# Optimization experiments

Measured on AMD Instinct MI355X. Metric: run time of the kernel, lower is better.

The kernel has to match this reference:

```python
import jax, jax.numpy as jnp
import numpy as np

IN_DIM, H1, H2, H3, LATENT = 1024, 1024, 512, 256, 256
D, K, BETA = 32, 2048, 0.25
B = 16384


def _leaky(x):
    return jax.nn.leaky_relu(x, negative_slope=0.01)


def setup_inputs() -> dict:
    key = jax.random.key(0)
    ks = jax.random.split(key, 18)
    def lin(k, fan_in, fan_out):
        kw, kb = jax.random.split(k)
        s = 1.0 / np.sqrt(fan_in)
        W = jax.random.uniform(kw, (fan_in, fan_out), jnp.float32, -s, s)
        b = jax.random.uniform(kb, (fan_out,), jnp.float32, -s, s)
        return W, b
    We1, be1 = lin(ks[0], IN_DIM, H1)
    We2, be2 = lin(ks[1], H1, H2)
    We3, be3 = lin(ks[2], H2, H3)
    We4, be4 = lin(ks[3], H3, LATENT)
    Wd1, bd1 = lin(ks[4], LATENT, H3)
    Wd2, bd2 = lin(ks[5], H3, H2)
    Wd3, bd3 = lin(ks[6], H2, H1)
    Wd4, bd4 = lin(ks[7], H1, IN_DIM)
    E = jax.random.uniform(ks[8], (K, D), jnp.float32, -1.0 / K, 1.0 / K)  # codebook
    x = jax.random.uniform(ks[9], (B, IN_DIM), jnp.float32)
    return {"x": x, "We1": We1, "be1": be1, "We2": We2, "be2": be2,
            "We3": We3, "be3": be3, "We4": We4, "be4": be4, "E": E,
            "Wd1": Wd1, "bd1": bd1, "Wd2": Wd2, "bd2": bd2,
            "Wd3": Wd3, "bd3": bd3, "Wd4": Wd4, "bd4": bd4}


def reference(x, We1, be1, We2, be2, We3, be3, We4, be4, E,
              Wd1, bd1, Wd2, bd2, Wd3, bd3, Wd4, bd4):
    # encoder MLP
    h = _leaky(x @ We1 + be1)
    h = _leaky(h @ We2 + be2)
    h = _leaky(h @ We3 + be3)
    z = h @ We4 + be4                      # [B, LATENT]
    # vector quantizer
    zr = z.reshape(-1, D)                  # [N, D], N = B*LATENT/D
    dist = (jnp.sum(zr * zr, axis=1, keepdims=True)
            + jnp.sum(E * E, axis=1)
            - 2.0 * zr @ E.T)              # [N, K]
    idx = jnp.argmin(dist, axis=1)         # [N]
    # one-hot @ E == direct gather of nearest codebook rows
    q = E[idx].reshape(z.shape)            # [B, LATENT]
    commit = jnp.mean(jnp.sum(jnp.square(jax.lax.stop_gradient(q) - z), axis=1))
    embed = jnp.mean(jnp.sum(jnp.square(q - jax.lax.stop_gradient(z)), axis=1))
    vq_loss = BETA * commit + embed
    e = z + jax.lax.stop_gradient(q - z)   # straight-through
    # decoder MLP
    h = _leaky(e @ Wd1 + bd1)
    h = _leaky(h @ Wd2 + bd2)
    h = _leaky(h @ Wd3 + bd3)
    recon = jax.nn.sigmoid(h @ Wd4 + bd4)
    recon_loss = jnp.mean(jnp.sum(jnp.square(recon - x), axis=-1))
    loss = recon_loss + vq_loss
    return z, e, recon, loss, recon_loss, vq_loss
```

## Files before the change

kernel.cpp:

```cpp
#include <hip/hip_runtime.h>
#include <stdint.h>

typedef __attribute__((ext_vector_type(8))) _Float16 half8;
typedef __attribute__((ext_vector_type(4))) _Float16 half4;
typedef __attribute__((ext_vector_type(4))) float f32x4;

__device__ __forceinline__ void gload_lds16(const void* g, void* l) {
  __builtin_amdgcn_global_load_lds(
      (const __attribute__((address_space(1))) void*)g,
      (__attribute__((address_space(3))) void*)l, 16, 0, 0);
}

#define GBAR asm volatile("s_barrier" ::: "memory")
#define LGKM0                                            \
  asm volatile("s_waitcnt lgkmcnt(0)" ::: "memory");     \
  __builtin_amdgcn_sched_barrier(0)

#define MMA_Q(QM, QN)                                                        \
  __builtin_amdgcn_s_setprio(1);                                             \
  _Pragma("unroll") for (int s = 0; s < 2; s++)                              \
  _Pragma("unroll") for (int i = 0; i < 4; i++)                              \
  _Pragma("unroll") for (int j = 0; j < 2; j++)                              \
      acc[(QM) * 4 + i][(QN) * 2 + j] = __builtin_amdgcn_mfma_f32_16x16x32_f16( \
          af[i][s], bq[j][s], acc[(QM) * 4 + i][(QN) * 2 + j], 0, 0, 0);     \
  __builtin_amdgcn_s_setprio(0);

template <int EPI>
__global__ __launch_bounds__(512, 2) void gemm8p(
    const _Float16* __restrict__ A, const _Float16* __restrict__ Bt,
    const float* __restrict__ bias, _Float16* __restrict__ Ch,
    float* __restrict__ Cf, int M, int N, int Kd,
    const _Float16* __restrict__ Xref, float* __restrict__ lossAcc) {
  extern __shared__ __align__(16) char dyn[];

  const int tid = threadIdx.x;
  const int lane = tid & 63;
  const int wav = tid >> 6;
  const int wr = wav >> 2;
  const int wc = wav & 3;
  const int l15 = lane & 15;
  const int quad = lane >> 4;

  const int nx = gridDim.x;
  const int nwg = nx * (int)gridDim.y;
  int bid = (int)blockIdx.y * nx + (int)blockIdx.x;
  bid = (bid & 7) * (nwg >> 3) + (bid >> 3);
  const int shift = 31 - __clz(nx);
  const int m0 = (bid >> shift) * 256;
  const int n0 = (bid & (nx - 1)) * 256;

  f32x4 acc[8][4];
#pragma unroll
  for (int i = 0; i < 8; i++)
#pragma unroll
    for (int j = 0; j < 4; j++) acc[i][j] = (f32x4){0.f, 0.f, 0.f, 0.f};

  auto stageA = [&](int kt, int slot, int RB) {
    const int row = RB + (tid >> 3);
    const int ch = tid & 7;
    const int gm = m0 + ((row >> 6) & 1) * 128 + (row >> 7) * 64 + (row & 63);
    const int kc = (ch ^ (row & 7)) << 3;
    gload_lds16(A + (size_t)gm * Kd + kt + kc,
                dyn + slot * 65536 + row * 128 + ch * 16);
  };
  auto stageB = [&](int kt, int slot, int RB) {
    const int row = RB + (tid >> 3);
    const int ch = tid & 7;
    const int gn = n0 + ((row >> 5) & 3) * 64 + (row >> 7) * 32 + (row & 31);
    const int kc = (ch ^ (row & 7)) << 3;
    gload_lds16(Bt + (size_t)gn * Kd + kt + kc,
                dyn + slot * 65536 + 32768 + row * 128 + ch * 16);
  };

  half8 af[4][2], bq[2][2];
  auto dsA = [&](const _Float16* As, int qm) {
#pragma unroll
    for (int i = 0; i < 4; i++) {
      const int ra = qm * 128 + wr * 64 + i * 16 + l15;
#pragma unroll
      for (int s = 0; s < 2; s++)
        af[i][s] = *(const half8*)&As[ra * 64 + (((s * 4 + quad) ^ (ra & 7)) << 3)];
    }
  };
  auto dsB = [&](const _Float16* Bs, int qn) {
#pragma unroll
    for (int j = 0; j < 2; j++) {
      const int rb = qn * 128 + wc * 32 + j * 16 + l15;
#pragma unroll
      for (int s = 0; s < 2; s++)
        bq[j][s] = *(const half8*)&Bs[rb * 64 + (((s * 4 + quad) ^ (rb & 7)) << 3)];
    }
  };

  const int NT = Kd >> 6;

  stageA(0, 0, 0);
  stageA(0, 0, 64);
  stageB(0, 0, 128);
  stageB(0, 0, 192);
  stageA(0, 0, 128);
  stageA(0, 0, 192);
  stageB(0, 0, 0);
  stageB(0, 0, 64);
  stageA(64, 1, 0);
  stageA(64, 1, 64);
  stageB(64, 1, 128);
  stageB(64, 1, 192);
  asm volatile("s_waitcnt vmcnt(4)" ::: "memory");
  GBAR;

  for (int t = 0; t < NT; ++t) {
    const int slot = t & 1;
    const int nsl = slot ^ 1;
    const int kt1 = (t + 1) << 6;
    const int kt2 = (t + 2) << 6;
    const bool p1 = (t + 1) < NT;
    const bool p2 = (t + 2) < NT;
    const _Float16* As = (const _Float16*)(dyn + slot * 65536);
    const _Float16* Bs = (const _Float16*)(dyn + slot * 65536 + 32768);

    dsA(As, 0);
    dsB(Bs, 0);
    if (p1) { stageA(kt1, nsl, 128); stageA(kt1, nsl, 192); }
    GBAR;
    LGKM0;
    MMA_Q(0, 0);
    GBAR;
    dsB(Bs, 1);
    if (p1) { stageB(kt1, nsl, 0); stageB(kt1, nsl, 64); }
    GBAR;
    LGKM0;
    MMA_Q(0, 1);
    GBAR;
    dsA(As, 1);
    if (p2) { stageA(kt2, slot, 0); stageA(kt2, slot, 64); }
    GBAR;
    LGKM0;
    MMA_Q(1, 1);
    GBAR;
    dsB(Bs, 0);
    if (p2) { stageB(kt2, slot, 128); stageB(kt2, slot, 192); }
    GBAR;
    LGKM0;
    MMA_Q(1, 0);
    if (p2) {
      asm volatile("s_waitcnt vmcnt(4)" ::: "memory");
    } else {
      asm volatile("s_waitcnt vmcnt(0)" ::: "memory");
    }
    GBAR;
  }

  float lsum = 0.f;
  float* eb = (float*)dyn;
  float* red = (float*)dyn + 64 * 256;
#pragma unroll
  for (int p = 0; p < 4; p++) {
    __syncthreads();
    if (wr == (p >> 1)) {
#pragma unroll
      for (int mi2 = 0; mi2 < 4; mi2++) {
        const int mi = (p & 1) * 4 + mi2;
#pragma unroll
        for (int ni = 0; ni < 4; ni++)
#pragma unroll
          for (int r = 0; r < 4; r++) {
            const int rl = mi2 * 16 + quad * 4 + r;
            const int cl = wc * 64 + ni * 16 + l15;
            eb[rl * 256 + cl] = acc[mi][ni][r];
          }
      }
    }
    __syncthreads();
#pragma unroll
    for (int j = 0; j < 8; j++) {
      const int c = j * 512 + tid;
      const int rl = c >> 6;
      const int cl = (c & 63) * 4;
      const f32x4 v = *(const f32x4*)&eb[rl * 256 + cl];
      const int gcol = n0 + cl;
      const f32x4 bv = *(const f32x4*)&bias[gcol];
      const size_t o = (size_t)(m0 + p * 64 + rl) * N + gcol;
      if (EPI == 0) {
        half4 h;
#pragma unroll
        for (int q = 0; q < 4; q++) {
          float tv = v[q] + bv[q];
          tv = tv > 0.f ? tv : 0.01f * tv;
          h[q] = (_Float16)tv;
        }
        *(half4*)&Ch[o] = h;
      } else {
        const half4 xr = *(const half4*)&Xref[o];
        f32x4 sv;
#pragma unroll
        for (int q = 0; q < 4; q++) {
          const float sg = 1.f / (1.f + __expf(-(v[q] + bv[q])));
          sv[q] = sg;
          const float d = sg - (float)xr[q];
          lsum += d * d;
        }
        *(f32x4*)&Cf[o] = sv;
      }
    }
  }
  if (EPI == 2) {
    __syncthreads();
    red[tid] = lsum;
    __syncthreads();
    for (int s = 256; s > 0; s >>= 1) {
      if (tid < s) red[tid] += red[tid + s];
      __syncthreads();
    }
    if (tid == 0) atomicAdd(lossAcc, red[0]);
  }
}

template <int EPI, int BM, int BN>
__global__ __launch_bounds__(256, ((BM + BN) >= 256 ? 2 : ((BM + BN) == 192 ? 3 : 4)))
void gemm_bt(
    const _Float16* __restrict__ A, const _Float16* __restrict__ Bt,
    const float* __restrict__ bias, _Float16* __restrict__ Ch,
    float* __restrict__ Cf, int M, int N, int Kd,
    const _Float16* __restrict__ Xref, float* __restrict__ lossAcc) {
  constexpr int WM = BM / 2, WN = BN / 2;
  constexpr int MF = WM / 16, NF = WN / 16;
  constexpr int CA = BM / 32, CB = BN / 32;
  constexpr int CHUNKS = CA + CB;
  constexpr int STAGE = (BM + BN) * 64;
  __shared__ __align__(16) _Float16 smem[2 * STAGE];
  float* red = (float*)smem + 64 * BN;

  const int tid = threadIdx.x;
  const int lane = tid & 63;
  const int wav = tid >> 6;
  const int nx = gridDim.x;
  const int nwg = nx * (int)gridDim.y;
  int bid = (int)blockIdx.y * nx + (int)blockIdx.x;
  bid = (bid & 7) * (nwg >> 3) + (bid >> 3);
  const int shift = 31 - __clz(nx);
  const int m0 = (bid >> shift) * BM;
  const int n0 = (bid & (nx - 1)) * BN;
  const int wm = (wav >> 1) * WM;
  const int wn = (wav & 1) * WN;
  const int l15 = lane & 15;
  const int quad = lane >> 4;

  f32x4 acc[MF][NF];
#pragma unroll
  for (int i = 0; i < MF; i++)
#pragma unroll
    for (int j = 0; j < NF; j++) acc[i][j] = (f32x4){0.f, 0.f, 0.f, 0.f};

  auto issue = [&](int kt, int b) {
    _Float16* As = smem + b * STAGE;
    _Float16* Bs = As + BM * 64;
#pragma unroll
    for (int j = 0; j < CA; j++) {
      const int ci = j * 256 + tid;
      const int row = ci >> 3;
      const int kc = ((ci & 7) ^ (row & 7)) << 3;
      gload_lds16(A + (size_t)(m0 + row) * Kd + kt + kc, &As[ci * 8]);
    }
#pragma unroll
    for (int j = 0; j < CB; j++) {
      const int ci = j * 256 + tid;
      const int row = ci >> 3;
      const int kc = ((ci & 7) ^ (row & 7)) << 3;
      gload_lds16(Bt + (size_t)(n0 + row) * Kd + kt + kc, &Bs[ci * 8]);
    }
  };

  int buf = 0;
  issue(0, 0);
  for (int kt = 0; kt < Kd; kt += 64) {
    if (kt + 64 < Kd) {
      issue(kt + 64, buf ^ 1);
      asm volatile("s_waitcnt vmcnt(%0)" ::"i"(CHUNKS) : "memory");
    } else {
      asm volatile("s_waitcnt vmcnt(0)" ::: "memory");
    }
    asm volatile("s_barrier" ::: "memory");

    const _Float16* As = smem + buf * STAGE;
    const _Float16* Bs = As + BM * 64;
#pragma unroll
    for (int s = 0; s < 2; s++) {
      half8 af[MF], bqv[NF];
#pragma unroll
      for (int i = 0; i < MF; i++) {
        const int ra = wm + i * 16 + l15;
        const int ca = (s * 4 + quad) ^ (ra & 7);
        af[i] = *(const half8*)&As[ra * 64 + ca * 8];
      }
#pragma unroll
      for (int i = 0; i < NF; i++) {
        const int rb = wn + i * 16 + l15;
        const int cb = (s * 4 + quad) ^ (rb & 7);
        bqv[i] = *(const half8*)&Bs[rb * 64 + cb * 8];
      }
#pragma unroll
      for (int mi = 0; mi < MF; mi++)
#pragma unroll
        for (int ni = 0; ni < NF; ni++)
          acc[mi][ni] = __builtin_amdgcn_mfma_f32_16x16x32_f16(af[mi], bqv[ni],
                                                               acc[mi][ni], 0, 0, 0);
    }
    asm volatile("s_barrier" ::: "memory");
    buf ^= 1;
  }

  float lsum = 0.f;
  float* eb = (float*)smem;
  constexpr int DIV = BN / 4;
#pragma unroll
  for (int p = 0; p < BM / 64; p++) {
    __syncthreads();
    if ((wm >> 6) == p) {
#pragma unroll
      for (int mi = 0; mi < MF; mi++)
#pragma unroll
        for (int ni = 0; ni < NF; ni++)
#pragma unroll
          for (int r = 0; r < 4; r++) {
            const int rl = (wm & 63) + mi * 16 + quad * 4 + r;
            const int cl = wn + ni * 16 + l15;
            eb[rl * BN + cl] = acc[mi][ni][r];
          }
    }
    __syncthreads();
#pragma unroll
    for (int j = 0; j < BN / 16; j++) {
      const int c = j * 256 + tid;
      const int rl = c / DIV;
      const int cl = (c % DIV) * 4;
      const f32x4 v = *(const f32x4*)&eb[rl * BN + cl];
      const int gcol = n0 + cl;
      const f32x4 bv = *(const f32x4*)&bias[gcol];
      const size_t o = (size_t)(m0 + p * 64 + rl) * N + gcol;
      if (EPI == 0) {
        half4 h;
#pragma unroll
        for (int q = 0; q < 4; q++) {
          float t = v[q] + bv[q];
          t = t > 0.f ? t : 0.01f * t;
          h[q] = (_Float16)t;
        }
        *(half4*)&Ch[o] = h;
      } else if (EPI == 1) {
        f32x4 t;
        half4 h;
#pragma unroll
        for (int q = 0; q < 4; q++) {
          t[q] = v[q] + bv[q];
          h[q] = (_Float16)t[q];
        }
        *(f32x4*)&Cf[o] = t;
        *(half4*)&Ch[o] = h;
      } else {
        const half4 xr = *(const half4*)&Xref[o];
        f32x4 sv;
#pragma unroll
        for (int q = 0; q < 4; q++) {
          const float s = 1.f / (1.f + __expf(-(v[q] + bv[q])));
          sv[q] = s;
          const float d = s - (float)xr[q];
          lsum += d * d;
        }
        *(f32x4*)&Cf[o] = sv;
      }
    }
  }
  if (EPI == 2) {
    __syncthreads();
    red[tid] = lsum;
    __syncthreads();
    for (int s = 128; s > 0; s >>= 1) {
      if (tid < s) red[tid] += red[tid + s];
      __syncthreads();
    }
    if (tid == 0) atomicAdd(lossAcc, red[0]);
  }
}

__global__ __launch_bounds__(256, 4) void vq_argmin(
    const _Float16* __restrict__ zh, const _Float16* __restrict__ Ehf,
    const float* __restrict__ E, const float* __restrict__ ek2,
    float* __restrict__ e_out, _Float16* __restrict__ eh_out,
    float* __restrict__ vq_acc) {
  __shared__ __align__(16) _Float16 Es[512 * 32];
  __shared__ float ek2s[512];
  __shared__ float z2s[128];
  __shared__ int idxs[128];
  __shared__ float vred[256];

  const int tid = threadIdx.x;
  const int lane = tid & 63;
  const int wav = tid >> 6;
  const int l15 = lane & 15;
  const int quad = lane >> 4;
  const int rbase = blockIdx.x * 128 + wav * 32;
  constexpr unsigned KEYMASK = 0xFFFFF800u;

  half8 zf[2];
  float z2p[2];
#pragma unroll
  for (int m = 0; m < 2; m++) {
    zf[m] = *(const half8*)(zh + ((size_t)(rbase + m * 16 + l15)) * 32 + quad * 8);
    float s = 0.f;
#pragma unroll
    for (int j = 0; j < 8; j++) {
      float v = (float)zf[m][j];
      s += v * v;
    }
    s += __shfl_xor(s, 16);
    s += __shfl_xor(s, 32);
    z2p[m] = s;
  }
  if (quad == 0) {
#pragma unroll
    for (int m = 0; m < 2; m++) z2s[wav * 32 + m * 16 + l15] = z2p[m];
  }

  float key[2][4];
#pragma unroll
  for (int m = 0; m < 2; m++)
#pragma unroll
    for (int r = 0; r < 4; r++) key[m][r] = 1e30f;

  for (int cb = 0; cb < 2048; cb += 512) {
    __syncthreads();
#pragma unroll
    for (int j = 0; j < 8; j++) {
      const int u = j * 256 + tid;
      gload_lds16(Ehf + (size_t)cb * 32 + u * 8, &Es[u * 8]);
    }
    if (tid < 128) gload_lds16(&ek2[cb + tid * 4], &ek2s[tid * 4]);
    __syncthreads();

    int idxv = cb + l15;
    for (int c16 = 0; c16 < 32; c16++) {
      const half8 ef = *(const half8*)&Es[(c16 * 64 + lane) * 8];
      const float e2 = ek2s[c16 * 16 + l15];
      const f32x4 cinit = (f32x4){e2, e2, e2, e2};
      f32x4 d0 = __builtin_amdgcn_mfma_f32_16x16x32_f16(zf[0], ef, cinit, 0, 0, 0);
      f32x4 d1 = __builtin_amdgcn_mfma_f32_16x16x32_f16(zf[1], ef, cinit, 0, 0, 0);
#pragma unroll
      for (int r = 0; r < 4; r++) {
        key[0][r] = fminf(key[0][r],
                          __uint_as_float((__float_as_uint(d0[r]) & KEYMASK) | idxv));
        key[1][r] = fminf(key[1][r],
                          __uint_as_float((__float_as_uint(d1[r]) & KEYMASK) | idxv));
      }
      idxv += 16;
    }
  }

#pragma unroll
  for (int off = 1; off < 16; off <<= 1)
#pragma unroll
    for (int m = 0; m < 2; m++)
#pragma unroll
      for (int r = 0; r < 4; r++)
        key[m][r] = fminf(key[m][r], __shfl_xor(key[m][r], off));

  float vpart = 0.f;
  if (l15 == 0) {
#pragma unroll
    for (int m = 0; m < 2; m++)
#pragma unroll
      for (int r = 0; r < 4; r++) {
        const unsigned kb = __float_as_uint(key[m][r]);
        const int rl = wav * 32 + m * 16 + quad * 4 + r;
        idxs[rl] = (int)(kb & 0x7FFu);
        vpart += z2s[rl] + __uint_as_float(kb & KEYMASK);
      }
  }
  vred[tid] = vpart;
  __syncthreads();
  for (int s = 128; s > 0; s >>= 1) {
    if (tid < s) vred[tid] += vred[tid + s];
    __syncthreads();
  }
  if (tid == 0) atomicAdd(vq_acc, vred[0]);

#pragma unroll
  for (int it = 0; it < 2; it++) {
    const int slot = it * 256 + tid;
    const int rowb = slot >> 2, part = slot & 3;
    const int idx = idxs[rowb];
    const size_t orow = ((size_t)blockIdx.x * 128 + rowb) * 32 + part * 8;
    const f32x4 ea = *(const f32x4*)(E + (size_t)idx * 32 + part * 8);
    const f32x4 ebv = *(const f32x4*)(E + (size_t)idx * 32 + part * 8 + 4);
    *(f32x4*)(e_out + orow) = ea;
    *(f32x4*)(e_out + orow + 4) = ebv;
    half8 ehv;
#pragma unroll
    for (int j = 0; j < 4; j++) {
      ehv[j] = (_Float16)ea[j];
      ehv[j + 4] = (_Float16)ebv[j];
    }
    *(half8*)(eh_out + orow) = ehv;
  }
}

struct PrepArgs {
  const float* W[8];
  _Float16* Wt[8];
  int Kw[8], Nw[8];
  int base[9];
  const float* x;
  _Float16* xh;
  const float* E;
  _Float16* Ehf;
  float* ek2;
};

__global__ __launch_bounds__(256) void prep_k(PrepArgs a) {
  __shared__ float t[32][33];
  const int b = blockIdx.x;
  const int tid = threadIdx.x;
  if (b < 8192) {
    const size_t i = (size_t)b * 256 + tid;
    const f32x4 va = *(const f32x4*)(a.x + i * 8);
    const f32x4 vb = *(const f32x4*)(a.x + i * 8 + 4);
    half8 h;
#pragma unroll
    for (int j = 0; j < 4; j++) {
      h[j] = (_Float16)va[j];
      h[j + 4] = (_Float16)vb[j];
    }
    *(half8*)(a.xh + i * 8) = h;
    return;
  }
  if (b < 8192 + 3456) {
    int l = b - 8192;
    int w = 0;
    while (l >= a.base[w + 1]) w++;
    l -= a.base[w];
    const float* W = a.W[w];
    _Float16* Wt = a.Wt[w];
    const int K = a.Kw[w], N = a.Nw[w];
    const int nb = N >> 5;
    const int bx = (l % nb) * 32, by = (l / nb) * 32;
    const int tx = tid & 31, ty = tid >> 5;
#pragma unroll
    for (int i = 0; i < 32; i += 8)
      t[ty + i][tx] = W[(size_t)(by + ty + i) * N + bx + tx];
    __syncthreads();
#pragma unroll
    for (int i = 0; i < 32; i += 8)
      Wt[(size_t)(bx + ty + i) * K + by + tx] = (_Float16)t[tx][ty + i];
    return;
  }
  const int c = (b - 8192 - 3456) * 256 + tid;
  float s = 0.f;
#pragma unroll
  for (int k = 0; k < 32; k++) {
    const float v = a.E[(size_t)c * 32 + k];
    s += v * v;
    a.Ehf[(size_t)((c >> 4) * 64 + (k >> 3) * 16 + (c & 15)) * 8 + (k & 7)] =
        (_Float16)(-2.f * v);
  }
  a.ek2[c] = s;
}

__global__ void finalize_k(const float* __restrict__ scal, float* __restrict__ out) {
  const float vq = 1.25f * (scal[0] / 16384.f);
  const float rl = scal[1] / 16384.f;
  out[0] = rl + vq;
  out[1] = rl;
  out[2] = vq;
}

extern "C" void kernel_launch(void* const* d_in, const int* in_sizes, int n_in,
                              void* d_out, int out_size, void* d_ws, size_t ws_size,
                              hipStream_t stream) {
  const float* x = (const float*)d_in[0];
  const float* be1 = (const float*)d_in[2];
  const float* be2 = (const float*)d_in[4];
  const float* be3 = (const float*)d_in[6];
  const float* be4 = (const float*)d_in[8];
  const float* E = (const float*)d_in[9];
  const float* bd1 = (const float*)d_in[11];
  const float* bd2 = (const float*)d_in[13];
  const float* bd3 = (const float*)d_in[15];
  const float* bd4 = (const float*)d_in[17];

  float* out = (float*)d_out;
  char* ws = (char*)d_ws;

  size_t off = 0;
  auto alloc = [&](size_t bytes) {
    size_t r = off;
    off += (bytes + 255) & ~(size_t)255;
    return r;
  };
  const size_t oXH = alloc((size_t)16384 * 1024 * 2);
  const size_t oWT1 = alloc((size_t)1024 * 1024 * 2);
  const size_t oWT2 = alloc((size_t)512 * 1024 * 2);
  const size_t oWT3 = alloc((size_t)256 * 512 * 2);
  const size_t oWT4 = alloc((size_t)256 * 256 * 2);
  const size_t oWD1 = alloc((size_t)256 * 256 * 2);
  const size_t oWD2 = alloc((size_t)512 * 256 * 2);
  const size_t oWD3 = alloc((size_t)1024 * 512 * 2);
  const size_t oWD4 = alloc((size_t)1024 * 1024 * 2);
  const size_t oEHF = alloc((size_t)2048 * 32 * 2);
  const size_t oEK2 = alloc((size_t)2048 * 4);
  const size_t oSC = alloc(256);
  const size_t oZH = alloc((size_t)16384 * 256 * 2);
  const size_t oQH = alloc((size_t)16384 * 256 * 2);
  const size_t oH1 = alloc((size_t)16384 * 1024 * 2);
  const size_t oH2 = alloc((size_t)16384 * 512 * 2);
  const size_t oH3 = alloc((size_t)16384 * 256 * 2);

  _Float16* xh = (_Float16*)(ws + oXH);
  _Float16* WT1 = (_Float16*)(ws + oWT1);
  _Float16* WT2 = (_Float16*)(ws + oWT2);
  _Float16* WT3 = (_Float16*)(ws + oWT3);
  _Float16* WT4 = (_Float16*)(ws + oWT4);
  _Float16* WD1 = (_Float16*)(ws + oWD1);
  _Float16* WD2 = (_Float16*)(ws + oWD2);
  _Float16* WD3 = (_Float16*)(ws + oWD3);
  _Float16* WD4 = (_Float16*)(ws + oWD4);
  _Float16* Ehf = (_Float16*)(ws + oEHF);
  float* ek2 = (float*)(ws + oEK2);
  float* scal = (float*)(ws + oSC);
  _Float16* zhw = (_Float16*)(ws + oZH);
  _Float16* qh = (_Float16*)(ws + oQH);
  _Float16* h1 = (_Float16*)(ws + oH1);
  _Float16* h2 = (_Float16*)(ws + oH2);
  _Float16* h3 = (_Float16*)(ws + oH3);

  float* zout = out;
  float* eout = out + (size_t)16384 * 256;
  float* rout = out + (size_t)16384 * 256 * 2;
  float* sout = rout + (size_t)16384 * 1024;

  hipMemsetAsync(ws + oSC, 0, 8, stream);

  hipFuncSetAttribute((const void*)gemm8p<0>,
                      hipFuncAttributeMaxDynamicSharedMemorySize, 131072);
  hipFuncSetAttribute((const void*)gemm8p<2>,
                      hipFuncAttributeMaxDynamicSharedMemorySize, 131072);

  PrepArgs pa;
  pa.W[0] = (const float*)d_in[1];  pa.Wt[0] = WT1; pa.Kw[0] = 1024; pa.Nw[0] = 1024;
  pa.W[1] = (const float*)d_in[3];  pa.Wt[1] = WT2; pa.Kw[1] = 1024; pa.Nw[1] = 512;
  pa.W[2] = (const float*)d_in[5];  pa.Wt[2] = WT3; pa.Kw[2] = 512;  pa.Nw[2] = 256;
  pa.W[3] = (const float*)d_in[7];  pa.Wt[3] = WT4; pa.Kw[3] = 256;  pa.Nw[3] = 256;
  pa.W[4] = (const float*)d_in[10]; pa.Wt[4] = WD1; pa.Kw[4] = 256;  pa.Nw[4] = 256;
  pa.W[5] = (const float*)d_in[12]; pa.Wt[5] = WD2; pa.Kw[5] = 256;  pa.Nw[5] = 512;
  pa.W[6] = (const float*)d_in[14]; pa.Wt[6] = WD3; pa.Kw[6] = 512;  pa.Nw[6] = 1024;
  pa.W[7] = (const float*)d_in[16]; pa.Wt[7] = WD4; pa.Kw[7] = 1024; pa.Nw[7] = 1024;
  int acc = 0;
  for (int w = 0; w < 8; w++) {
    pa.base[w] = acc;
    acc += (pa.Kw[w] >> 5) * (pa.Nw[w] >> 5);
  }
  pa.base[8] = acc;
  pa.x = x; pa.xh = xh; pa.E = E; pa.Ehf = Ehf; pa.ek2 = ek2;

  dim3 blk(256);
  prep_k<<<8192 + 3456 + 8, blk, 0, stream>>>(pa);

  gemm8p<0><<<dim3(4, 64), dim3(512), 131072, stream>>>(
      xh, WT1, be1, h1, nullptr, 16384, 1024, 1024, nullptr, nullptr);
  gemm_bt<0, 128, 128><<<dim3(4, 128), blk, 0, stream>>>(
      h1, WT2, be2, h2, nullptr, 16384, 512, 1024, nullptr, nullptr);
  gemm_bt<0, 64, 64><<<dim3(4, 256), blk, 0, stream>>>(
      h2, WT3, be3, h3, nullptr, 16384, 256, 512, nullptr, nullptr);
  gemm_bt<1, 64, 64><<<dim3(4, 256), blk, 0, stream>>>(
      h3, WT4, be4, zhw, zout, 16384, 256, 256, nullptr, nullptr);
  vq_argmin<<<1024, blk, 0, stream>>>(zhw, Ehf, E, ek2, eout, qh, &scal[0]);
  gemm_bt<0, 64, 64><<<dim3(4, 256), blk, 0, stream>>>(
      qh, WD1, bd1, h3, nullptr, 16384, 256, 256, nullptr, nullptr);
  gemm_bt<0, 128, 128><<<dim3(4, 128), blk, 0, stream>>>(
      h3, WD2, bd2, h2, nullptr, 16384, 512, 256, nullptr, nullptr);
  gemm8p<0><<<dim3(4, 64), dim3(512), 131072, stream>>>(
      h2, WD3, bd3, h1, nullptr, 16384, 1024, 512, nullptr, nullptr);
  gemm8p<2><<<dim3(4, 64), dim3(512), 131072, stream>>>(
      h1, WD4, bd4, nullptr, rout, 16384, 1024, 1024, xh, &scal[1]);
  finalize_k<<<1, 1, 0, stream>>>(scal, sout);
}
```

Baseline: 381.7 us.

## Reorder GEMM prefetch stages, peel last K-iteration, and prefetch Xref during final MMAs

Changes the order in which A and B quarter-tiles are staged into LDS so more loads stay in flight (vmcnt 6 instead of 4), and peels the final K iteration out of the main loop. In the peeled iteration, for the sigmoid/loss epilogue, the reference input tiles are loaded into registers while the last MFMAs run, so the epilogue no longer waits on those global loads. This uses 32 extra half4 registers per thread, which raises register pressure and may lower occupancy.

```diff
diff --git a/kernel.cpp b/kernel.cpp
--- a/kernel.cpp
+++ b/kernel.cpp
@@ -94,60 +94,116 @@
 
   const int NT = Kd >> 6;
 
+  half4 xp[4][8];
+
   stageA(0, 0, 0);
   stageA(0, 0, 64);
-  stageB(0, 0, 128);
-  stageB(0, 0, 192);
   stageA(0, 0, 128);
   stageA(0, 0, 192);
   stageB(0, 0, 0);
   stageB(0, 0, 64);
+  stageB(0, 0, 128);
+  stageB(0, 0, 192);
   stageA(64, 1, 0);
   stageA(64, 1, 64);
   stageB(64, 1, 128);
   stageB(64, 1, 192);
-  asm volatile("s_waitcnt vmcnt(4)" ::: "memory");
+  stageA(64, 1, 128);
+  stageA(64, 1, 192);
+  asm volatile("s_waitcnt vmcnt(6)" ::: "memory");
   GBAR;
 
-  for (int t = 0; t < NT; ++t) {
+  for (int t = 0; t < NT - 1; ++t) {
     const int slot = t & 1;
     const int nsl = slot ^ 1;
     const int kt1 = (t + 1) << 6;
     const int kt2 = (t + 2) << 6;
-    const bool p1 = (t + 1) < NT;
-    const bool p2 = (t + 2) < NT;
+    const bool s2 = (t + 2) < NT;
     const _Float16* As = (const _Float16*)(dyn + slot * 65536);
     const _Float16* Bs = (const _Float16*)(dyn + slot * 65536 + 32768);
 
     dsA(As, 0);
     dsB(Bs, 0);
-    if (p1) { stageA(kt1, nsl, 128); stageA(kt1, nsl, 192); }
+    stageB(kt1, nsl, 0);
+    stageB(kt1, nsl, 64);
     GBAR;
     LGKM0;
     MMA_Q(0, 0);
     GBAR;
     dsB(Bs, 1);
-    if (p1) { stageB(kt1, nsl, 0); stageB(kt1, nsl, 64); }
+    if (s2) { stageA(kt2, slot, 0); stageA(kt2, slot, 64); }
     GBAR;
     LGKM0;
     MMA_Q(0, 1);
     GBAR;
     dsA(As, 1);
-    if (p2) { stageA(kt2, slot, 0); stageA(kt2, slot, 64); }
+    if (s2) { stageB(kt2, slot, 128); stageB(kt2, slot, 192); }
     GBAR;
     LGKM0;
     MMA_Q(1, 1);
     GBAR;
     dsB(Bs, 0);
-    if (p2) { stageB(kt2, slot, 128); stageB(kt2, slot, 192); }
+    if (s2) { stageA(kt2, slot, 128); stageA(kt2, slot, 192); }
     GBAR;
     LGKM0;
     MMA_Q(1, 0);
-    if (p2) {
-      asm volatile("s_waitcnt vmcnt(4)" ::: "memory");
+    if (s2) {
+      asm volatile("s_waitcnt vmcnt(6)" ::: "memory");
     } else {
       asm volatile("s_waitcnt vmcnt(0)" ::: "memory");
     }
+    GBAR;
+  }
+
+  {
+    const int slot = (NT - 1) & 1;
+    const _Float16* As = (const _Float16*)(dyn + slot * 65536);
+    const _Float16* Bs = (const _Float16*)(dyn + slot * 65536 + 32768);
+    const size_t xbase = (size_t)m0 * N + n0 + (size_t)wav * N + lane * 4;
+
+    dsA(As, 0);
+    dsB(Bs, 0);
+    if (EPI == 2) {
+#pragma unroll
+      for (int j = 0; j < 8; j++)
+        xp[0][j] = *(const half4*)&Xref[xbase + (size_t)(0 * 64 + j * 8) * N];
+    }
+    GBAR;
+    LGKM0;
+    MMA_Q(0, 0);
+    GBAR;
+
+    dsB(Bs, 1);
+    if (EPI == 2) {
+#pragma unroll
+      for (int j = 0; j < 8; j++)
+        xp[1][j] = *(const half4*)&Xref[xbase + (size_t)(1 * 64 + j * 8) * N];
+    }
+    GBAR;
+    LGKM0;
+    MMA_Q(0, 1);
+    GBAR;
+
+    dsA(As, 1);
+    if (EPI == 2) {
+#pragma unroll
+      for (int j = 0; j < 8; j++)
+        xp[2][j] = *(const half4*)&Xref[xbase + (size_t)(2 * 64 + j * 8) * N];
+    }
+    GBAR;
+    LGKM0;
+    MMA_Q(1, 1);
+    GBAR;
+
+    dsB(Bs, 0);
+    if (EPI == 2) {
+#pragma unroll
+      for (int j = 0; j < 8; j++)
+        xp[3][j] = *(const half4*)&Xref[xbase + (size_t)(3 * 64 + j * 8) * N];
+    }
+    GBAR;
+    LGKM0;
+    MMA_Q(1, 0);
     GBAR;
   }
 
@@ -191,7 +247,7 @@
         }
         *(half4*)&Ch[o] = h;
       } else {
-        const half4 xr = *(const half4*)&Xref[o];
+        const half4 xr = xp[p][j];
         f32x4 sv;
 #pragma unroll
         for (int q = 0; q < 4; q++) {
```

Measured after the change: 384.9 us. Within noise of the previous version (+0.8%).

## Deepen the GEMM prefetch schedule and store the sigmoid epilogue directly from registers

Applied to the files above, without the earlier changes.

The staged global-to-LDS loads are reordered so that more of the next-next K tile is issued earlier. The wait threshold rises from vmcnt(4) to vmcnt(6), which leaves more loads in flight behind the MFMA quarters. For the final sigmoid/loss GEMM, the epilogue no longer stages accumulators through LDS with per-pass barriers: each lane applies bias and sigmoid, then writes its fragment values straight to global memory and reads X in place. This removes LDS traffic and synchronisation, but in exchange it uses narrower, less coalesced scalar stores and loads, and it relies on the new per-fragment column mapping being correct.

```diff
diff --git a/kernel.cpp b/kernel.cpp
--- a/kernel.cpp
+++ b/kernel.cpp
@@ -96,17 +96,19 @@
 
   stageA(0, 0, 0);
   stageA(0, 0, 64);
-  stageB(0, 0, 128);
-  stageB(0, 0, 192);
   stageA(0, 0, 128);
   stageA(0, 0, 192);
   stageB(0, 0, 0);
   stageB(0, 0, 64);
+  stageB(0, 0, 128);
+  stageB(0, 0, 192);
   stageA(64, 1, 0);
   stageA(64, 1, 64);
   stageB(64, 1, 128);
   stageB(64, 1, 192);
-  asm volatile("s_waitcnt vmcnt(4)" ::: "memory");
+  stageA(64, 1, 128);
+  stageA(64, 1, 192);
+  asm volatile("s_waitcnt vmcnt(6)" ::: "memory");
   GBAR;
 
   for (int t = 0; t < NT; ++t) {
@@ -115,104 +117,115 @@
     const int kt1 = (t + 1) << 6;
     const int kt2 = (t + 2) << 6;
     const bool p1 = (t + 1) < NT;
-    const bool p2 = (t + 2) < NT;
+    const bool s2 = (t + 2) < NT;
     const _Float16* As = (const _Float16*)(dyn + slot * 65536);
     const _Float16* Bs = (const _Float16*)(dyn + slot * 65536 + 32768);
 
     dsA(As, 0);
     dsB(Bs, 0);
-    if (p1) { stageA(kt1, nsl, 128); stageA(kt1, nsl, 192); }
+    if (p1) { stageB(kt1, nsl, 0); stageB(kt1, nsl, 64); }
     GBAR;
     LGKM0;
     MMA_Q(0, 0);
     GBAR;
     dsB(Bs, 1);
-    if (p1) { stageB(kt1, nsl, 0); stageB(kt1, nsl, 64); }
+    if (s2) { stageA(kt2, slot, 0); stageA(kt2, slot, 64); }
     GBAR;
     LGKM0;
     MMA_Q(0, 1);
     GBAR;
     dsA(As, 1);
-    if (p2) { stageA(kt2, slot, 0); stageA(kt2, slot, 64); }
+    if (s2) { stageB(kt2, slot, 128); stageB(kt2, slot, 192); }
     GBAR;
     LGKM0;
     MMA_Q(1, 1);
     GBAR;
     dsB(Bs, 0);
-    if (p2) { stageB(kt2, slot, 128); stageB(kt2, slot, 192); }
+    if (s2) { stageA(kt2, slot, 128); stageA(kt2, slot, 192); }
     GBAR;
     LGKM0;
     MMA_Q(1, 0);
-    if (p2) {
-      asm volatile("s_waitcnt vmcnt(4)" ::: "memory");
+    if (s2) {
+      asm volatile("s_waitcnt vmcnt(6)" ::: "memory");
     } else {
       asm volatile("s_waitcnt vmcnt(0)" ::: "memory");
     }
     GBAR;
   }
 
-  float lsum = 0.f;
-  float* eb = (float*)dyn;
-  float* red = (float*)dyn + 64 * 256;
-#pragma unroll
-  for (int p = 0; p < 4; p++) {
-    __syncthreads();
-    if (wr == (p >> 1)) {
-#pragma unroll
-      for (int mi2 = 0; mi2 < 4; mi2++) {
-        const int mi = (p & 1) * 4 + mi2;
-#pragma unroll
-        for (int ni = 0; ni < 4; ni++)
-#pragma unroll
-          for (int r = 0; r < 4; r++) {
-            const int rl = mi2 * 16 + quad * 4 + r;
-            const int cl = wc * 64 + ni * 16 + l15;
-            eb[rl * 256 + cl] = acc[mi][ni][r];
-          }
-      }
-    }
-    __syncthreads();
-#pragma unroll
-    for (int j = 0; j < 8; j++) {
-      const int c = j * 512 + tid;
-      const int rl = c >> 6;
-      const int cl = (c & 63) * 4;
-      const f32x4 v = *(const f32x4*)&eb[rl * 256 + cl];
-      const int gcol = n0 + cl;
-      const f32x4 bv = *(const f32x4*)&bias[gcol];
-      const size_t o = (size_t)(m0 + p * 64 + rl) * N + gcol;
-      if (EPI == 0) {
+  if (EPI == 2) {
+    float lsum = 0.f;
+    int colv[4];
+    float bv[4];
+#pragma unroll
+    for (int ni = 0; ni < 4; ni++) {
+      colv[ni] = n0 + wc * 64 + (ni >> 1) * 32 + (ni & 1) * 16 + l15;
+      bv[ni] = bias[colv[ni]];
+    }
+    const int gr0 = m0 + wr * 128;
+#pragma unroll
+    for (int mi = 0; mi < 8; mi++) {
+      const int row = gr0 + (mi >> 2) * 64 + (mi & 3) * 16 + quad * 4;
+#pragma unroll
+      for (int r = 0; r < 4; r++) {
+        const size_t ro = (size_t)(row + r) * N;
+#pragma unroll
+        for (int ni = 0; ni < 4; ni++) {
+          const size_t o = ro + colv[ni];
+          const float sg = 1.f / (1.f + __expf(-(acc[mi][ni][r] + bv[ni])));
+          Cf[o] = sg;
+          const float d = sg - (float)Xref[o];
+          lsum += d * d;
+        }
+      }
+    }
+    float* red = (float*)dyn;
+    red[tid] = lsum;
+    __syncthreads();
+    for (int s = 256; s > 0; s >>= 1) {
+      if (tid < s) red[tid] += red[tid + s];
+      __syncthreads();
+    }
+    if (tid == 0) atomicAdd(lossAcc, red[0]);
+  } else {
+    float* eb = (float*)dyn;
+#pragma unroll
+    for (int p = 0; p < 4; p++) {
+      __syncthreads();
+      if (wr == (p >> 1)) {
+#pragma unroll
+        for (int mi2 = 0; mi2 < 4; mi2++) {
+          const int mi = (p & 1) * 4 + mi2;
+#pragma unroll
+          for (int ni = 0; ni < 4; ni++)
+#pragma unroll
+            for (int r = 0; r < 4; r++) {
+              const int rl = mi2 * 16 + quad * 4 + r;
+              const int cl = wc * 64 + ni * 16 + l15;
+              eb[rl * 256 + cl] = acc[mi][ni][r];
+            }
+        }
+      }
+      __syncthreads();
+#pragma unroll
+      for (int j = 0; j < 8; j++) {
+        const int c = j * 512 + tid;
+        const int rl = c >> 6;
+        const int cl = (c & 63) * 4;
+        const f32x4 v = *(const f32x4*)&eb[rl * 256 + cl];
+        const int gcol = n0 + cl;
+        const f32x4 bvv = *(const f32x4*)&bias[gcol];
+        const size_t o = (size_t)(m0 + p * 64 + rl) * N + gcol;
         half4 h;
 #pragma unroll
         for (int q = 0; q < 4; q++) {
-          float tv = v[q] + bv[q];
+          float tv = v[q] + bvv[q];
           tv = tv > 0.f ? tv : 0.01f * tv;
           h[q] = (_Float16)tv;
         }
         *(half4*)&Ch[o] = h;
-      } else {
-        const half4 xr = *(const half4*)&Xref[o];
-        f32x4 sv;
-#pragma unroll
-        for (int q = 0; q < 4; q++) {
-          const float sg = 1.f / (1.f + __expf(-(v[q] + bv[q])));
-          sv[q] = sg;
-          const float d = sg - (float)xr[q];
-          lsum += d * d;
-        }
-        *(f32x4*)&Cf[o] = sv;
-      }
-    }
-  }
-  if (EPI == 2) {
-    __syncthreads();
-    red[tid] = lsum;
-    __syncthreads();
-    for (int s = 256; s > 0; s >>= 1) {
-      if (tid < s) red[tid] += red[tid + s];
-      __syncthreads();
-    }
-    if (tid == 0) atomicAdd(lossAcc, red[0]);
+      }
+    }
   }
 }
 
```

Result: slower. 396.0 us (+3.7%).
